# Performance work log

Hardware: AMD Instinct MI355X
Metric: run time of the kernel (lower is better)

The kernel has to match this reference:

```python
import jax, jax.numpy as jnp
import numpy as np
import math

D_MODEL = 1024
NUM_HEADS = 16
D_K = D_MODEL // NUM_HEADS


def setup_inputs() -> dict:
    key = jax.random.key(0)
    ks = jax.random.split(key, 5)
    scale = 1.0 / math.sqrt(D_MODEL)
    x = jax.random.normal(ks[0], (2, 2048, D_MODEL), dtype=jnp.float32)
    qkv_w = jax.random.uniform(ks[1], (3 * D_MODEL, D_MODEL), jnp.float32, -scale, scale)
    qkv_b = jax.random.uniform(ks[2], (3 * D_MODEL,), jnp.float32, -scale, scale)
    out_w = jax.random.uniform(ks[3], (D_MODEL, D_MODEL), jnp.float32, -scale, scale)
    out_b = jax.random.uniform(ks[4], (D_MODEL,), jnp.float32, -scale, scale)
    return {"x": x, "qkv_w": qkv_w, "qkv_b": qkv_b, "out_w": out_w, "out_b": out_b}


def reference(x, qkv_w, qkv_b, out_w, out_b):
    B, N, D = x.shape
    # fused QKV projection (torch Linear: x @ W.T + b)
    qkv = x @ qkv_w.T + qkv_b                       # (B, N, 3D)
    qkv = qkv.reshape(B, N, 3, NUM_HEADS, D_K)
    qkv = jnp.transpose(qkv, (2, 0, 3, 1, 4))        # (3, B, H, N, d_k)
    q, k, v = qkv[0], qkv[1], qkv[2]
    attn = jnp.einsum('bhnd,bhmd->bhnm', q, k) / math.sqrt(D_K)  # (B,H,N,N)
    attn = jax.nn.softmax(attn, axis=-1)
    out = jnp.einsum('bhnm,bhmd->bhnd', attn, v)     # (B,H,N,d_k)
    out = jnp.transpose(out, (0, 2, 1, 3)).reshape(B, N, D)
    return out @ out_w.T + out_b
```

## Files before the change

### kernel.cpp

```cpp
#include <hip/hip_runtime.h>
#include <hip/hip_bf16.h>


typedef __bf16 bf16x8 __attribute__((ext_vector_type(8)));
typedef __bf16 bf16x4 __attribute__((ext_vector_type(4)));
typedef short short4v __attribute__((ext_vector_type(4)));
typedef float f32x4 __attribute__((ext_vector_type(4)));
typedef float f32x16 __attribute__((ext_vector_type(16)));

#define QSCALE 0.18033688011112042f

__device__ __forceinline__ unsigned short bfbits(float f) {
    union { __bf16 h; unsigned short u; } cv;
    cv.h = (__bf16)f;
    return cv.u;
}

__device__ __forceinline__ f32x4 mfma16(bf16x4 a, bf16x4 b, f32x4 c) {
#if __has_builtin(__builtin_amdgcn_mfma_f32_16x16x16bf16_1k)
    union { bf16x4 h; short4v s; } ua, ub;
    ua.h = a; ub.h = b;
    return __builtin_amdgcn_mfma_f32_16x16x16bf16_1k(ua.s, ub.s, c, 0, 0, 0);
#else
    f32x4 d = c;
    asm volatile("v_mfma_f32_16x16x16_bf16 %0, %1, %2, %0"
                 : "+v"(d) : "v"(a), "v"(b));
    return d;
#endif
}

__device__ __forceinline__ void gl_lds16(const void* g, void* l) {
    __builtin_amdgcn_global_load_lds(
        (__attribute__((address_space(1))) const unsigned int*)g,
        (__attribute__((address_space(3))) unsigned int*)l, 16, 0, 0);
}

__global__ void cvt_all(const float4* __restrict__ x,
                        const float4* __restrict__ wq,
                        const float4* __restrict__ wo,
                        ushort4* __restrict__ d0,
                        ushort4* __restrict__ d1,
                        ushort4* __restrict__ d2) {
    int i = blockIdx.x * blockDim.x + threadIdx.x;
    const int stride = gridDim.x * blockDim.x;
    for (; i < 2097152; i += stride) {
        float4 f;
        ushort4* d;
        int k;
        if (i < 1048576)       { f = x[i];           d = d0; k = i; }
        else if (i < 1835008)  { f = wq[i - 1048576]; d = d1; k = i - 1048576; }
        else                   { f = wo[i - 1835008]; d = d2; k = i - 1835008; }
        ushort4 o;
        o.x = bfbits(f.x); o.y = bfbits(f.y); o.z = bfbits(f.z); o.w = bfbits(f.w);
        d[k] = o;
    }
}

template<int MODE>
__global__ __launch_bounds__(256, 3) void gemm_mfma(
    const unsigned short* __restrict__ A,
    const unsigned short* __restrict__ W,
    const float* __restrict__ bias,
    unsigned short* __restrict__ qo,
    unsigned short* __restrict__ ko,
    unsigned short* __restrict__ vto,
    float* __restrict__ fo) {
    __shared__ __attribute__((aligned(128))) unsigned char smem[32768];
    const int lane = threadIdx.x & 63;
    const int w = threadIdx.x >> 6;
    const int c5 = lane & 31, hi = lane >> 5;
    const int wr = w >> 1, wc = w & 1;
    const int row0 = blockIdx.x * 128;
    const int col0 = blockIdx.y * 128;

    const int rloc = lane >> 3;
    const int csrc = ((lane & 7) ^ rloc) * 8;

    f32x16 acc[2][2] = {};

    const int ra = wr * 64 + c5;
    const int rb = wc * 64 + c5;
    const int swa = ra & 7, swb = rb & 7;

    for (int kt = 0; kt < 1024; kt += 64) {
        #pragma unroll
        for (int i = 0; i < 4; ++i) {
            const int r = i * 32 + w * 8 + rloc;
            gl_lds16(A + (size_t)(row0 + r) * 1024 + kt + csrc,
                     smem + i * 4096 + w * 1024);
            gl_lds16(W + (size_t)(col0 + r) * 1024 + kt + csrc,
                     smem + 16384 + i * 4096 + w * 1024);
        }
        __syncthreads();

        #pragma unroll
        for (int ks = 0; ks < 4; ++ks) {
            const int ch_a = ((2 * ks + hi) ^ swa) * 16;
            const int ch_b = ((2 * ks + hi) ^ swb) * 16;
            bf16x8 a0 = *(const bf16x8*)(smem + ra * 128 + ch_a);
            bf16x8 a1 = *(const bf16x8*)(smem + (ra + 32) * 128 + ch_a);
            bf16x8 b0 = *(const bf16x8*)(smem + 16384 + rb * 128 + ch_b);
            bf16x8 b1 = *(const bf16x8*)(smem + 16384 + (rb + 32) * 128 + ch_b);
            acc[0][0] = __builtin_amdgcn_mfma_f32_32x32x16_bf16(a0, b0, acc[0][0], 0, 0, 0);
            acc[0][1] = __builtin_amdgcn_mfma_f32_32x32x16_bf16(a0, b1, acc[0][1], 0, 0, 0);
            acc[1][0] = __builtin_amdgcn_mfma_f32_32x32x16_bf16(a1, b0, acc[1][0], 0, 0, 0);
            acc[1][1] = __builtin_amdgcn_mfma_f32_32x32x16_bf16(a1, b1, acc[1][1], 0, 0, 0);
        }
        __syncthreads();
    }

    #pragma unroll
    for (int mi = 0; mi < 2; ++mi) {
        #pragma unroll
        for (int ni = 0; ni < 2; ++ni) {
            const int col = col0 + wc * 64 + ni * 32 + c5;
            const float bv = bias[col];
            #pragma unroll
            for (int r = 0; r < 16; ++r) {
                const int row = row0 + wr * 64 + mi * 32 + (r & 3) + 8 * (r >> 2) + 4 * hi;
                float v = acc[mi][ni][r] + bv;
                if (MODE == 1) {
                    fo[(size_t)row * 1024 + col] = v;
                } else {
                    const int sec = col >> 10;
                    const int d = col & 1023;
                    const int h = d >> 6, dk = d & 63;
                    const int b_ = row >> 11, n = row & 2047;
                    const int bh = b_ * 16 + h;
                    if (sec == 0)
                        qo[((size_t)(bh * 2048 + n) << 6) + dk] = bfbits(v * QSCALE);
                    else if (sec == 1)
                        ko[((size_t)(bh * 2048 + n) << 6) + dk] = bfbits(v);
                    else
                        vto[(size_t)(bh * 64 + dk) * 2048 + n] = bfbits(v);
                }
            }
        }
    }
}

__global__ __launch_bounds__(512, 4) void attn_flash(
    const unsigned short* __restrict__ Q,
    const unsigned short* __restrict__ K,
    const unsigned short* __restrict__ Vt,
    unsigned short* __restrict__ O) {
    __shared__ __attribute__((aligned(128))) unsigned char smem[65536];
    const int lane = threadIdx.x & 63;
    const int w = threadIdx.x >> 6;
    const int hw = w & 3;
    const int hz = w >> 2;
    const int g = lane >> 4, c = lane & 15;
    const int c7 = c & 7;

    const int d = blockIdx.x + 16 * blockIdx.y;
    const int wv = (d & 7) * 64 + (d >> 3);
    const int bx = wv & 15;
    const int bh = wv >> 4;

    const int q0 = bx * 128 + hw * 32;
    const unsigned short* Qb = Q + (size_t)bh * 2048 * 64;
    const unsigned short* Kb = K + (size_t)bh * 2048 * 64;
    const unsigned short* Vb = Vt + (size_t)bh * 64 * 2048;

    const int rloc = lane >> 3;
    const int csrc = ((lane & 7) ^ (rloc & 7)) * 8;

    const int chunkKV0 = ((0 + g) ^ c7) * 16;
    const int chunkKV1 = ((4 + g) ^ c7) * 16;
    const int ghalf = g >> 1;
    const int gsub = (g & 1) * 8;

    unsigned char* Sbase = smem + hz * 32768;

    bf16x8 aq[2][2];
    #pragma unroll
    for (int qg = 0; qg < 2; ++qg)
        #pragma unroll
        for (int ks = 0; ks < 2; ++ks)
            aq[qg][ks] = *(const bf16x8*)(Qb + (size_t)(q0 + qg * 16 + c) * 64 + ks * 32 + 8 * g);

    f32x4 oa[4] = {}, ob[4] = {};
    f32x4 la = {}, lb = {};
    float ma = -1e30f, mb = -1e30f;

    bf16x4 ones4;
    #pragma unroll
    for (int i = 0; i < 4; ++i) ones4[i] = (__bf16)1.0f;

    const int gt0 = hz * 16;

    #pragma unroll
    for (int tt = 0; tt < 2; ++tt) {
        const int t = 2 * hw + tt;
        const int row = 8 * t + rloc;
        gl_lds16(Kb + (size_t)(gt0 * 64 + row) * 64 + csrc, Sbase + t * 1024);
        gl_lds16(Vb + (size_t)row * 2048 + gt0 * 64 + csrc, Sbase + 16384 + t * 1024);
    }
    __syncthreads();

    for (int t = 0; t < 16; ++t) {
        const int cur = t & 1;
        if (t + 1 < 16) {
            const int nb = cur ^ 1;
            const int gt = gt0 + t + 1;
            #pragma unroll
            for (int tt = 0; tt < 2; ++tt) {
                const int ti = 2 * hw + tt;
                const int row = 8 * ti + rloc;
                gl_lds16(Kb + (size_t)(gt * 64 + row) * 64 + csrc,
                         Sbase + nb * 8192 + ti * 1024);
                gl_lds16(Vb + (size_t)row * 2048 + gt * 64 + csrc,
                         Sbase + 16384 + nb * 8192 + ti * 1024);
            }
        }

        const unsigned char* Kt = Sbase + cur * 8192;
        const unsigned char* Vtb = Sbase + 16384 + cur * 8192;

        f32x4 sa[4] = {}, sb[4] = {};
        __builtin_amdgcn_s_setprio(1);
        #pragma unroll
        for (int nj = 0; nj < 4; ++nj) {
            bf16x8 bk0 = *(const bf16x8*)(Kt + nj * 2048 + c * 128 + chunkKV0);
            bf16x8 bk1 = *(const bf16x8*)(Kt + nj * 2048 + c * 128 + chunkKV1);
            sa[nj] = __builtin_amdgcn_mfma_f32_16x16x32_bf16(bk0, aq[0][0], sa[nj], 0, 0, 0);
            sa[nj] = __builtin_amdgcn_mfma_f32_16x16x32_bf16(bk1, aq[0][1], sa[nj], 0, 0, 0);
            sb[nj] = __builtin_amdgcn_mfma_f32_16x16x32_bf16(bk0, aq[1][0], sb[nj], 0, 0, 0);
            sb[nj] = __builtin_amdgcn_mfma_f32_16x16x32_bf16(bk1, aq[1][1], sb[nj], 0, 0, 0);
        }
        __builtin_amdgcn_s_setprio(0);

        float pa, pb;
        {
            float a0 = fmaxf(fmaxf(sa[0][0], sa[0][1]), fmaxf(sa[0][2], sa[0][3]));
            float a1 = fmaxf(fmaxf(sa[1][0], sa[1][1]), fmaxf(sa[1][2], sa[1][3]));
            float a2 = fmaxf(fmaxf(sa[2][0], sa[2][1]), fmaxf(sa[2][2], sa[2][3]));
            float a3 = fmaxf(fmaxf(sa[3][0], sa[3][1]), fmaxf(sa[3][2], sa[3][3]));
            pa = fmaxf(fmaxf(a0, a1), fmaxf(a2, a3));
            float b0 = fmaxf(fmaxf(sb[0][0], sb[0][1]), fmaxf(sb[0][2], sb[0][3]));
            float b1 = fmaxf(fmaxf(sb[1][0], sb[1][1]), fmaxf(sb[1][2], sb[1][3]));
            float b2 = fmaxf(fmaxf(sb[2][0], sb[2][1]), fmaxf(sb[2][2], sb[2][3]));
            float b3 = fmaxf(fmaxf(sb[3][0], sb[3][1]), fmaxf(sb[3][2], sb[3][3]));
            pb = fmaxf(fmaxf(b0, b1), fmaxf(b2, b3));
        }

        const bool trig = (pa > ma + 8.f) || (pb > mb + 8.f);
        if (__any((int)trig)) {
            float rm = pa;
            rm = fmaxf(rm, __shfl_xor(rm, 16));
            rm = fmaxf(rm, __shfl_xor(rm, 32));
            float mnew = fmaxf(ma, rm);
            float sc = __builtin_amdgcn_exp2f(ma - mnew);
            ma = mnew;
            #pragma unroll
            for (int j = 0; j < 4; ++j) {
                const float scj = __shfl(sc, 4 * g + j);
                la[j] *= scj;
                #pragma unroll
                for (int ni = 0; ni < 4; ++ni) oa[ni][j] *= scj;
            }
            rm = pb;
            rm = fmaxf(rm, __shfl_xor(rm, 16));
            rm = fmaxf(rm, __shfl_xor(rm, 32));
            mnew = fmaxf(mb, rm);
            sc = __builtin_amdgcn_exp2f(mb - mnew);
            mb = mnew;
            #pragma unroll
            for (int j = 0; j < 4; ++j) {
                const float scj = __shfl(sc, 4 * g + j);
                lb[j] *= scj;
                #pragma unroll
                for (int ni = 0; ni < 4; ++ni) ob[ni][j] *= scj;
            }
        }

        bf16x4 qa_[4], qb_[4];
        #pragma unroll
        for (int nj = 0; nj < 4; ++nj)
            #pragma unroll
            for (int j = 0; j < 4; ++j) {
                qa_[nj][j] = (__bf16)__builtin_amdgcn_exp2f(sa[nj][j] - ma);
                qb_[nj][j] = (__bf16)__builtin_amdgcn_exp2f(sb[nj][j] - mb);
            }

        f32x4 lta = {}, ltb = {};
        __builtin_amdgcn_s_setprio(1);
        #pragma unroll
        for (int nj = 0; nj < 4; ++nj) {
            lta = mfma16(qa_[nj], ones4, lta);
            ltb = mfma16(qb_[nj], ones4, ltb);
            #pragma unroll
            for (int ni = 0; ni < 4; ++ni) {
                bf16x4 bv = *(const bf16x4*)(Vtb + (ni * 16 + c) * 128 +
                                             (((2 * nj + ghalf) ^ c7) * 16) + gsub);
                oa[ni] = mfma16(qa_[nj], bv, oa[ni]);
                ob[ni] = mfma16(qb_[nj], bv, ob[ni]);
            }
        }
        __builtin_amdgcn_s_setprio(0);
        la += lta;
        lb += ltb;

        __syncthreads();
    }

    f32x4 mja, mjb;
    #pragma unroll
    for (int j = 0; j < 4; ++j) {
        mja[j] = __shfl(ma, 4 * g + j);
        mjb[j] = __shfl(mb, 4 * g + j);
    }

    unsigned char* xbuf = smem + hw * 12288;
    if (hz == 1) {
        #pragma unroll
        for (int ni = 0; ni < 4; ++ni) {
            *(f32x4*)(xbuf + ni * 1024 + lane * 16) = oa[ni];
            *(f32x4*)(xbuf + (4 + ni) * 1024 + lane * 16) = ob[ni];
        }
        *(f32x4*)(xbuf + 8192 + 0 * 1024 + lane * 16) = mja;
        *(f32x4*)(xbuf + 8192 + 1 * 1024 + lane * 16) = la;
        *(f32x4*)(xbuf + 8192 + 2 * 1024 + lane * 16) = mjb;
        *(f32x4*)(xbuf + 8192 + 3 * 1024 + lane * 16) = lb;
    }
    __syncthreads();

    if (hz == 0) {
        f32x4 poa[4], pob[4];
        #pragma unroll
        for (int ni = 0; ni < 4; ++ni) {
            poa[ni] = *(const f32x4*)(xbuf + ni * 1024 + lane * 16);
            pob[ni] = *(const f32x4*)(xbuf + (4 + ni) * 1024 + lane * 16);
        }
        const f32x4 pmja = *(const f32x4*)(xbuf + 8192 + 0 * 1024 + lane * 16);
        const f32x4 pla  = *(const f32x4*)(xbuf + 8192 + 1 * 1024 + lane * 16);
        const f32x4 pmjb = *(const f32x4*)(xbuf + 8192 + 2 * 1024 + lane * 16);
        const f32x4 plb  = *(const f32x4*)(xbuf + 8192 + 3 * 1024 + lane * 16);

        const int b_ = bh >> 4, h = bh & 15;
        #pragma unroll
        for (int j = 0; j < 4; ++j) {
            {
                const float mx = fmaxf(mja[j], pmja[j]);
                const float e0 = __builtin_amdgcn_exp2f(mja[j] - mx);
                const float e1 = __builtin_amdgcn_exp2f(pmja[j] - mx);
                const float inv = 1.f / (e0 * la[j] + e1 * pla[j]);
                const int row = b_ * 2048 + q0 + 4 * g + j;
                #pragma unroll
                for (int ni = 0; ni < 4; ++ni) {
                    const int col = h * 64 + ni * 16 + c;
                    O[(size_t)row * 1024 + col] =
                        bfbits((e0 * oa[ni][j] + e1 * poa[ni][j]) * inv);
                }
            }
            {
                const float mx = fmaxf(mjb[j], pmjb[j]);
                const float e0 = __builtin_amdgcn_exp2f(mjb[j] - mx);
                const float e1 = __builtin_amdgcn_exp2f(pmjb[j] - mx);
                const float inv = 1.f / (e0 * lb[j] + e1 * plb[j]);
                const int row = b_ * 2048 + q0 + 16 + 4 * g + j;
                #pragma unroll
                for (int ni = 0; ni < 4; ++ni) {
                    const int col = h * 64 + ni * 16 + c;
                    O[(size_t)row * 1024 + col] =
                        bfbits((e0 * ob[ni][j] + e1 * pob[ni][j]) * inv);
                }
            }
        }
    }
}

extern "C" void kernel_launch(void* const* d_in, const int* in_sizes, int n_in,
                              void* d_out, int out_size, void* d_ws, size_t ws_size,
                              hipStream_t stream) {
    const float* x     = (const float*)d_in[0];
    const float* qkv_w = (const float*)d_in[1];
    const float* qkv_b = (const float*)d_in[2];
    const float* out_w = (const float*)d_in[3];
    const float* out_b = (const float*)d_in[4];
    float* out = (float*)d_out;

    char* ws = (char*)d_ws;
    unsigned short* xb   = (unsigned short*)(ws);
    unsigned short* wqkv = (unsigned short*)(ws + (8u  << 20));
    unsigned short* qb   = (unsigned short*)(ws + (16u << 20));
    unsigned short* kb   = (unsigned short*)(ws + (24u << 20));
    unsigned short* vtb  = (unsigned short*)(ws + (32u << 20));
    unsigned short* wout = (unsigned short*)(ws + (40u << 20));

    cvt_all<<<2048, 256, 0, stream>>>((const float4*)x, (const float4*)qkv_w,
                                      (const float4*)out_w,
                                      (ushort4*)xb, (ushort4*)wqkv, (ushort4*)wout);

    gemm_mfma<0><<<dim3(32, 24), 256, 0, stream>>>(xb, wqkv, qkv_b, qb, kb, vtb, nullptr);

    unsigned short* ao = xb;
    attn_flash<<<dim3(16, 32), 512, 0, stream>>>(qb, kb, vtb, ao);

    gemm_mfma<1><<<dim3(32, 8), 256, 0, stream>>>(ao, wout, out_b, nullptr, nullptr, nullptr, out);
}
```

Before: 120.2 us.

## Fuse x fp32-to-bf16 conversion into QKV GEMM loads and remap block order

The separate conversion of activations x to bf16 is removed. The QKV GEMM now reads fp32 x directly, converts it in registers and stores it swizzled into LDS, while the weight conversion stays in a smaller kernel. This saves a write and read of the bf16 x buffer and shrinks the conversion kernel. In exchange the A-operand loads move from async global-to-LDS transfers to synchronous register loads of twice as many bytes. A block-index remap also spreads consecutive blocks across column tiles, which may help L2 locality.

```diff
diff --git a/kernel.cpp b/kernel.cpp
--- a/kernel.cpp
+++ b/kernel.cpp
@@ -35,21 +35,18 @@
         (__attribute__((address_space(3))) unsigned int*)l, 16, 0, 0);
 }
 
-__global__ void cvt_all(const float4* __restrict__ x,
-                        const float4* __restrict__ wq,
-                        const float4* __restrict__ wo,
-                        ushort4* __restrict__ d0,
-                        ushort4* __restrict__ d1,
-                        ushort4* __restrict__ d2) {
+__global__ void cvt_w(const float4* __restrict__ wq,
+                      const float4* __restrict__ wo,
+                      ushort4* __restrict__ d1,
+                      ushort4* __restrict__ d2) {
     int i = blockIdx.x * blockDim.x + threadIdx.x;
     const int stride = gridDim.x * blockDim.x;
-    for (; i < 2097152; i += stride) {
+    for (; i < 1048576; i += stride) {
         float4 f;
         ushort4* d;
         int k;
-        if (i < 1048576)       { f = x[i];           d = d0; k = i; }
-        else if (i < 1835008)  { f = wq[i - 1048576]; d = d1; k = i - 1048576; }
-        else                   { f = wo[i - 1835008]; d = d2; k = i - 1835008; }
+        if (i < 786432) { f = wq[i];          d = d1; k = i; }
+        else            { f = wo[i - 786432]; d = d2; k = i - 786432; }
         ushort4 o;
         o.x = bfbits(f.x); o.y = bfbits(f.y); o.z = bfbits(f.z); o.w = bfbits(f.w);
         d[k] = o;
@@ -58,7 +55,8 @@
 
 template<int MODE>
 __global__ __launch_bounds__(256, 3) void gemm_mfma(
-    const unsigned short* __restrict__ A,
+    const float* __restrict__ Af,
+    const unsigned short* __restrict__ Ab,
     const unsigned short* __restrict__ W,
     const float* __restrict__ bias,
     unsigned short* __restrict__ qo,
@@ -70,8 +68,12 @@
     const int w = threadIdx.x >> 6;
     const int c5 = lane & 31, hi = lane >> 5;
     const int wr = w >> 1, wc = w & 1;
-    const int row0 = blockIdx.x * 128;
-    const int col0 = blockIdx.y * 128;
+
+    const int nb = gridDim.x * gridDim.y;
+    const int d = blockIdx.x + (blockIdx.y << 5);
+    const int wv = (d & 7) * (nb >> 3) + (d >> 3);
+    const int row0 = (wv & 31) * 128;
+    const int col0 = (wv >> 5) * 128;
 
     const int rloc = lane >> 3;
     const int csrc = ((lane & 7) ^ rloc) * 8;
@@ -86,8 +88,20 @@
         #pragma unroll
         for (int i = 0; i < 4; ++i) {
             const int r = i * 32 + w * 8 + rloc;
-            gl_lds16(A + (size_t)(row0 + r) * 1024 + kt + csrc,
-                     smem + i * 4096 + w * 1024);
+            if (MODE == 0) {
+                const float* src = Af + (size_t)(row0 + r) * 1024 + kt + (lane & 7) * 8;
+                const float4 f0 = *(const float4*)(src);
+                const float4 f1 = *(const float4*)(src + 4);
+                bf16x8 v;
+                v[0] = (__bf16)f0.x; v[1] = (__bf16)f0.y;
+                v[2] = (__bf16)f0.z; v[3] = (__bf16)f0.w;
+                v[4] = (__bf16)f1.x; v[5] = (__bf16)f1.y;
+                v[6] = (__bf16)f1.z; v[7] = (__bf16)f1.w;
+                *(bf16x8*)(smem + i * 4096 + (w * 8 + rloc) * 128 + csrc * 2) = v;
+            } else {
+                gl_lds16(Ab + (size_t)(row0 + r) * 1024 + kt + csrc,
+                         smem + i * 4096 + w * 1024);
+            }
             gl_lds16(W + (size_t)(col0 + r) * 1024 + kt + csrc,
                      smem + 16384 + i * 4096 + w * 1024);
         }
@@ -123,8 +137,8 @@
                     fo[(size_t)row * 1024 + col] = v;
                 } else {
                     const int sec = col >> 10;
-                    const int d = col & 1023;
-                    const int h = d >> 6, dk = d & 63;
+                    const int dd = col & 1023;
+                    const int h = dd >> 6, dk = dd & 63;
                     const int b_ = row >> 11, n = row & 2047;
                     const int bh = b_ * 16 + h;
                     if (sec == 0)
@@ -381,21 +395,21 @@
     float* out = (float*)d_out;
 
     char* ws = (char*)d_ws;
-    unsigned short* xb   = (unsigned short*)(ws);
+    unsigned short* ao   = (unsigned short*)(ws);
     unsigned short* wqkv = (unsigned short*)(ws + (8u  << 20));
     unsigned short* qb   = (unsigned short*)(ws + (16u << 20));
     unsigned short* kb   = (unsigned short*)(ws + (24u << 20));
     unsigned short* vtb  = (unsigned short*)(ws + (32u << 20));
     unsigned short* wout = (unsigned short*)(ws + (40u << 20));
 
-    cvt_all<<<2048, 256, 0, stream>>>((const float4*)x, (const float4*)qkv_w,
-                                      (const float4*)out_w,
-                                      (ushort4*)xb, (ushort4*)wqkv, (ushort4*)wout);
-
-    gemm_mfma<0><<<dim3(32, 24), 256, 0, stream>>>(xb, wqkv, qkv_b, qb, kb, vtb, nullptr);
-
-    unsigned short* ao = xb;
+    cvt_w<<<1024, 256, 0, stream>>>((const float4*)qkv_w, (const float4*)out_w,
+                                    (ushort4*)wqkv, (ushort4*)wout);
+
+    gemm_mfma<0><<<dim3(32, 24), 256, 0, stream>>>(x, nullptr, wqkv, qkv_b,
+                                                   qb, kb, vtb, nullptr);
+
     attn_flash<<<dim3(16, 32), 512, 0, stream>>>(qb, kb, vtb, ao);
 
-    gemm_mfma<1><<<dim3(32, 8), 256, 0, stream>>>(ao, wout, out_b, nullptr, nullptr, nullptr, out);
-}
+    gemm_mfma<1><<<dim3(32, 8), 256, 0, stream>>>(nullptr, ao, wout, out_b,
+                                                  nullptr, nullptr, nullptr, out);
+}
```

New measurement: 145.9 us. 1.21x slower.
